# Kernel optimization log

Hardware: AMD Instinct MI355X
Metric: run time of the kernel (lower is better)

Reference implementation:

```python
import jax, jax.numpy as jnp
import numpy as np

B, S, P, V, E, H = 64, 1024, 32, 32000, 128, 256


def _lstm_dir(x, Wih, Whh, b, reverse):
    # x: [S, B, E] -> hidden states [S, B, H]; PyTorch LSTM gate order i,f,g,o
    Bsz = x.shape[1]
    Hd = Whh.shape[1]

    def step(carry, xt):
        h, c = carry
        z = xt @ Wih.T + h @ Whh.T + b
        i, f, g, o = jnp.split(z, 4, axis=-1)
        i = jax.nn.sigmoid(i)
        f = jax.nn.sigmoid(f)
        g = jnp.tanh(g)
        o = jax.nn.sigmoid(o)
        c = f * c + i * g
        h = o * jnp.tanh(c)
        return (h, c), h

    init = (jnp.zeros((Bsz, Hd), x.dtype), jnp.zeros((Bsz, Hd), x.dtype))
    _, hs = jax.lax.scan(step, init, x, reverse=reverse)
    return hs


def setup_inputs():
    key = jax.random.key(0)
    ks = jax.random.split(key, 12)
    input_ids = jax.random.randint(ks[0], (B, S), 0, V)
    attention_mask = jnp.ones((B, S), jnp.int32)
    # token j covers chars [4j, 4j+4)
    starts = jnp.arange(S) * 4
    offset_mapping = jnp.broadcast_to(jnp.stack([starts, starts + 4], -1), (B, S, 2))
    # spans: contiguous token runs of 1..64 tokens, expressed as char offsets
    t0 = jax.random.randint(ks[1], (B, P), 0, S - 64)
    ln = jax.random.randint(ks[2], (B, P), 1, 64)
    positions = jnp.stack([t0 * 4, (t0 + ln) * 4], -1)
    sc = 0.05
    embedding = (jax.random.normal(ks[3], (V, E)) * sc).at[0].set(0.0)  # padding_idx=0
    Wih_f = jax.random.normal(ks[4], (4 * H, E)) * sc
    Whh_f = jax.random.normal(ks[5], (4 * H, H)) * sc
    bih_f = jnp.zeros((4 * H,))
    bhh_f = jnp.zeros((4 * H,))
    Wih_b = jax.random.normal(ks[6], (4 * H, E)) * sc
    Whh_b = jax.random.normal(ks[7], (4 * H, H)) * sc
    bih_b = jnp.zeros((4 * H,))
    bhh_b = jnp.zeros((4 * H,))
    fc_w = jax.random.normal(ks[8], (1, 2 * H)) * sc
    fc_b = jnp.zeros((1,))
    return dict(embedding=embedding, Wih_f=Wih_f, Whh_f=Whh_f, bih_f=bih_f, bhh_f=bhh_f,
                Wih_b=Wih_b, Whh_b=Whh_b, bih_b=bih_b, bhh_b=bhh_b, fc_w=fc_w, fc_b=fc_b,
                input_ids=input_ids, attention_mask=attention_mask,
                offset_mapping=offset_mapping, positions=positions)


def reference(embedding, Wih_f, Whh_f, bih_f, bhh_f, Wih_b, Whh_b, bih_b, bhh_b,
              fc_w, fc_b, input_ids, attention_mask, offset_mapping, positions):
    x = embedding[input_ids]              # [B,S,E]
    xt = jnp.swapaxes(x, 0, 1)            # [S,B,E]
    h_f = _lstm_dir(xt, Wih_f, Whh_f, bih_f + bhh_f, False)
    h_b = _lstm_dir(xt, Wih_b, Whh_b, bih_b + bhh_b, True)
    lstm_out = jnp.swapaxes(jnp.concatenate([h_f, h_b], -1), 0, 1)  # [B,S,2H]

    off_s = offset_mapping[..., 0]        # [B,S]
    off_e = offset_mapping[..., 1]
    pos_s = positions[..., 0]             # [B,P]
    pos_e = positions[..., 1]
    # token j belongs to span p iff s_j >= start_p and e_j <= end_p
    mask = (off_s[:, None, :] >= pos_s[:, :, None]) & (off_e[:, None, :] <= pos_e[:, :, None])
    m = mask.astype(lstm_out.dtype)       # [B,P,S]
    cnt = m.sum(-1)                       # [B,P]
    reps = jnp.einsum('bps,bsd->bpd', m, lstm_out) / jnp.maximum(cnt, 1.0)[..., None]
    valid = (cnt > 0) & ~((pos_s == 0) & (pos_e == 0))
    reps = jnp.where(valid[..., None], reps, 0.0)
    logits = reps @ fc_w.T + fc_b         # [B,P,1]
    return logits.squeeze(-1)
```

## Files before the change

kernel.cpp:

```cpp
#include <hip/hip_runtime.h>

#define S_  1024
#define B_  64
#define P_  32

typedef _Float16 f16;
typedef unsigned int u32;
typedef _Float16 half2_t __attribute__((ext_vector_type(2)));
typedef _Float16 half8_t __attribute__((ext_vector_type(8)));

__device__ __forceinline__ float dot8(half8_t w, half8_t h, float acc) {
#if __has_builtin(__builtin_amdgcn_fdot2)
    acc = __builtin_amdgcn_fdot2((half2_t){w[0], w[1]}, (half2_t){h[0], h[1]}, acc, false);
    acc = __builtin_amdgcn_fdot2((half2_t){w[2], w[3]}, (half2_t){h[2], h[3]}, acc, false);
    acc = __builtin_amdgcn_fdot2((half2_t){w[4], w[5]}, (half2_t){h[4], h[5]}, acc, false);
    acc = __builtin_amdgcn_fdot2((half2_t){w[6], w[7]}, (half2_t){h[6], h[7]}, acc, false);
#else
    #pragma unroll
    for (int j = 0; j < 8; ++j) acc += (float)w[j] * (float)h[j];
#endif
    return acc;
}

__device__ __forceinline__ float fast_sig(float x)  { return 1.f / (1.f + __expf(-x)); }
__device__ __forceinline__ float fast_tanh(float x) { return 1.f - 2.f / (1.f + __expf(2.f * x)); }

__global__ void k_prep_w(const float* __restrict__ wih_f, const float* __restrict__ whh_f,
                         const float* __restrict__ bih_f, const float* __restrict__ bhh_f,
                         const float* __restrict__ wih_b, const float* __restrict__ whh_b,
                         const float* __restrict__ bih_b, const float* __restrict__ bhh_b,
                         f16* __restrict__ Wreg, f16* __restrict__ Wlds,
                         float* __restrict__ bias2) {
    int rowg = blockIdx.x;
    int dir = rowg >> 10;
    int r = rowg & 1023;
    int col = threadIdx.x;
    int g = r >> 8, rem = r & 255, half = rem >> 7, up = rem & 127;
    int rid = g * 128 + up;
    const float* wih = dir ? wih_b : wih_f;
    const float* whh = dir ? whh_b : whh_f;
    if (col < 128) {
        float v = wih[r * 128 + col];
        Wreg[((((size_t)(dir * 2 + half) * 2 + 0) * 16 + (col >> 3)) * 512 + rid) * 8 + (col & 7)] = (f16)v;
    } else {
        int k = col - 128;
        float v = whh[r * 256 + k];
        int hc = k >> 7, kk = k & 127, c = kk >> 3, j = kk & 7;
        if (hc == half)
            Wreg[((((size_t)(dir * 2 + half) * 2 + 1) * 16 + c) * 512 + rid) * 8 + j] = (f16)v;
        else
            Wlds[(((size_t)(dir * 2 + half) * 16 + c) * 512 + rid) * 8 + j] = (f16)v;
    }
    if (col == 0) {
        const float* bi = dir ? bih_b : bih_f;
        const float* bh = dir ? bhh_b : bhh_f;
        bias2[rowg] = bi[r] + bh[r];
    }
}

__global__ void k_gather(const int* __restrict__ ids, const float* __restrict__ emb,
                         f16* __restrict__ X) {
    int m = blockIdx.x * 2 + (threadIdx.x >> 7);
    int k = threadIdx.x & 127;
    int id = ids[m];
    X[(size_t)m * 128 + k] = (f16)emb[(size_t)id * 128 + k];
}

__global__ void k_zero(u32* __restrict__ flags) {
    flags[threadIdx.x] = 0u;
}

__global__ __launch_bounds__(512, 1) void k_lstm(
        const f16* __restrict__ Wreg,
        const f16* __restrict__ Wlds,
        const float* __restrict__ bias2,
        const f16* __restrict__ X,
        const float* __restrict__ fcw,
        f16* __restrict__ Hx,
        u32* __restrict__ flags,
        float* __restrict__ Svp) {
    __shared__ __align__(16) f16 sh_w[16 * 512 * 8];
    __shared__ __align__(16) f16 sh_h[256];
    __shared__ float zbuf[4][128];

    const int blk  = blockIdx.x;
    const int dir  = blk >> 7;
    const int half = (blk >> 6) & 1;
    const int b    = blk & 63;
    const int tid  = threadIdx.x;
    const int g    = tid >> 7;
    const int up   = tid & 127;
    const int row  = g * 256 + half * 128 + up;

    const half8_t* wrg = (const half8_t*)Wreg;
    const size_t base_x = (((size_t)(dir * 2 + half) * 2 + 0) * 16) * 512 + tid;
    const size_t base_h = (((size_t)(dir * 2 + half) * 2 + 1) * 16) * 512 + tid;
    half8_t wx[16], wh[16];
    #pragma unroll
    for (int c = 0; c < 16; ++c) wx[c] = wrg[base_x + (size_t)c * 512];
    #pragma unroll
    for (int c = 0; c < 16; ++c) wh[c] = wrg[base_h + (size_t)c * 512];

    {
        const half8_t* wlg = (const half8_t*)Wlds + ((size_t)(dir * 2 + half) * 16) * 512 + tid;
        half8_t* shw = (half8_t*)sh_w;
        #pragma unroll
        for (int c = 0; c < 16; ++c) shw[c * 512 + tid] = wlg[(size_t)c * 512];
    }

    const float bias = bias2[dir * 1024 + row];

    const f16* Xb = X + (size_t)b * S_ * 128;
    const int fidx_own = (dir * 64 + b) * 2 + half;
    const int fidx_par = fidx_own ^ 1;
    f16*       hx_own = Hx + (size_t)fidx_own * 2 * 128;
    const f16* hx_par = Hx + (size_t)fidx_par * 2 * 128;

    float c0 = 0.f, c1 = 0.f, fc0 = 0.f, fc1 = 0.f;
    if (tid < 64) {
        fc0 = fcw[dir * 256 + half * 128 + 2 * tid];
        fc1 = fcw[dir * 256 + half * 128 + 2 * tid + 1];
    }

    if (tid < 128) ((u32*)sh_h)[tid] = 0u;
    __syncthreads();

    const half8_t* shh = (const half8_t*)sh_h;
    const half8_t* shw = (const half8_t*)sh_w;
    const int ownc = half * 16;
    const int parc = (1 - half) * 16;

    for (int s = 0; s < S_; ++s) {
        const int t = dir ? (S_ - 1 - s) : s;
        const half8_t* xrow = (const half8_t*)&Xb[(size_t)t * 128];

        float a0 = 0.f, a1 = 0.f, a2 = 0.f, a3 = 0.f;

        #pragma unroll
        for (int c = 0; c < 16; c += 2) {
            a0 = dot8(wh[c],     shh[ownc + c],     a0);
            a1 = dot8(wh[c + 1], shh[ownc + c + 1], a1);
        }
        #pragma unroll
        for (int c = 0; c < 16; c += 2) {
            a2 = dot8(wx[c],     xrow[c],     a2);
            a3 = dot8(wx[c + 1], xrow[c + 1], a3);
        }

        if (s > 0 && tid < 64) {
            if (tid == 0) {
                while (__hip_atomic_load(&flags[fidx_par], __ATOMIC_ACQUIRE,
                                         __HIP_MEMORY_SCOPE_AGENT) < (u32)s)
                    __builtin_amdgcn_s_sleep(1);
            }
            if (tid < 16)
                *(half8_t*)&sh_h[(1 - half) * 128 + tid * 8] =
                    *(const half8_t*)&hx_par[(size_t)(s & 1) * 128 + tid * 8];
        }
        __syncthreads();

        #pragma unroll
        for (int c = 0; c < 16; c += 2) {
            half8_t w0 = shw[c * 512 + tid];
            half8_t w1 = shw[(c + 1) * 512 + tid];
            a0 = dot8(w0, shh[parc + c],     a0);
            a1 = dot8(w1, shh[parc + c + 1], a1);
        }

        float z = a0 + a1 + a2 + a3 + bias;
        float act = (g == 2) ? fast_tanh(z) : fast_sig(z);
        zbuf[g][up] = act;
        __syncthreads();

        if (tid < 64) {
            const int u0 = 2 * tid, u1 = u0 + 1;
            float i0 = zbuf[0][u0], f0 = zbuf[1][u0], g0 = zbuf[2][u0], o0 = zbuf[3][u0];
            float i1 = zbuf[0][u1], f1 = zbuf[1][u1], g1 = zbuf[2][u1], o1 = zbuf[3][u1];
            c0 = f0 * c0 + i0 * g0;
            c1 = f1 * c1 + i1 * g1;
            float h0 = o0 * fast_tanh(c0);
            float h1 = o1 * fast_tanh(c1);
            f16 h0h = (f16)h0, h1h = (f16)h1;
            u32 packed = (u32)__builtin_bit_cast(unsigned short, h0h)
                       | ((u32)__builtin_bit_cast(unsigned short, h1h) << 16);
            ((u32*)&sh_h[half * 128])[tid] = packed;
            ((u32*)&hx_own[(size_t)((s + 1) & 1) * 128])[tid] = packed;
            float ps = h0 * fc0 + h1 * fc1;
            #pragma unroll
            for (int off = 32; off > 0; off >>= 1) ps += __shfl_down(ps, off);
            if (tid == 0) {
                __hip_atomic_store(&flags[fidx_own], (u32)(s + 1), __ATOMIC_RELEASE,
                                   __HIP_MEMORY_SCOPE_AGENT);
                Svp[(((size_t)half * 2 + dir) * 64 + b) * S_ + t] = ps;
            }
        }
        __syncthreads();
    }
}

__global__ __launch_bounds__(256) void k_pool(const float* __restrict__ Svp,
                                              const int* __restrict__ om,
                                              const int* __restrict__ pos,
                                              const float* __restrict__ fcb,
                                              float* __restrict__ out) {
    __shared__ float red[4][2];
    int bp = blockIdx.x;
    int b = bp >> 5, p = bp & 31;
    int ps = pos[(b * P_ + p) * 2];
    int pe = pos[(b * P_ + p) * 2 + 1];
    int tid = threadIdx.x;
    float sum = 0.f, cnt = 0.f;
    for (int j = tid; j < S_; j += 256) {
        int os = om[((size_t)b * S_ + j) * 2];
        int oe = om[((size_t)b * S_ + j) * 2 + 1];
        if (os >= ps && oe <= pe) {
            size_t base = (size_t)b * S_ + j;
            sum += Svp[0 * 65536 + base] + Svp[1 * 65536 + base]
                 + Svp[2 * 65536 + base] + Svp[3 * 65536 + base];
            cnt += 1.f;
        }
    }
    #pragma unroll
    for (int off = 32; off > 0; off >>= 1) {
        sum += __shfl_down(sum, off);
        cnt += __shfl_down(cnt, off);
    }
    if ((tid & 63) == 0) { red[tid >> 6][0] = sum; red[tid >> 6][1] = cnt; }
    __syncthreads();
    if (tid == 0) {
        sum = red[0][0] + red[1][0] + red[2][0] + red[3][0];
        cnt = red[0][1] + red[1][1] + red[2][1] + red[3][1];
        bool valid = (cnt > 0.f) && !(ps == 0 && pe == 0);
        float v = valid ? (sum / fmaxf(cnt, 1.f)) : 0.f;
        out[b * P_ + p] = v + fcb[0];
    }
}

extern "C" void kernel_launch(void* const* d_in, const int* in_sizes, int n_in,
                              void* d_out, int out_size, void* d_ws, size_t ws_size,
                              hipStream_t stream) {
    const float* emb   = (const float*)d_in[0];
    const float* wih_f = (const float*)d_in[1];
    const float* whh_f = (const float*)d_in[2];
    const float* bih_f = (const float*)d_in[3];
    const float* bhh_f = (const float*)d_in[4];
    const float* wih_b = (const float*)d_in[5];
    const float* whh_b = (const float*)d_in[6];
    const float* bih_b = (const float*)d_in[7];
    const float* bhh_b = (const float*)d_in[8];
    const float* fc_w  = (const float*)d_in[9];
    const float* fc_b  = (const float*)d_in[10];
    const int* ids     = (const int*)d_in[11];
    const int* om      = (const int*)d_in[13];
    const int* pos     = (const int*)d_in[14];

    char* ws = (char*)d_ws;
    f16*   X     = (f16*)(ws + 0);
    f16*   Wreg  = (f16*)(ws + 16777216);
    f16*   Wlds  = (f16*)(ws + 17825792);
    float* bias2 = (float*)(ws + 18350080);
    f16*   Hx    = (f16*)(ws + 18358272);
    u32*   flags = (u32*)(ws + 18489344);
    float* Svp   = (float*)(ws + 18490368);
    float* out   = (float*)d_out;

    k_prep_w<<<2048, 384, 0, stream>>>(wih_f, whh_f, bih_f, bhh_f,
                                       wih_b, whh_b, bih_b, bhh_b, Wreg, Wlds, bias2);
    k_gather<<<32768, 256, 0, stream>>>(ids, emb, X);
    k_zero<<<1, 256, 0, stream>>>(flags);
    k_lstm<<<256, 512, 0, stream>>>(Wreg, Wlds, bias2, X, fc_w, Hx, flags, Svp);
    k_pool<<<2048, 256, 0, stream>>>(Svp, om, pos, fc_b, out);
}
```

Before: 8.117 ms.

## Split LSTM gate dot products across 1024 threads and batch input projections per 32 steps

Each block now runs 1024 threads, with each pair of threads splitting the K dimension of a gate row. All recurrent weights are held in registers, so the LDS weight copy goes away. The input projection W_x·x_t is computed in chunks of 32 timesteps into an LDS buffer stored as fp16, which takes the x loads and the dot products off the per-step critical path. The cost is an extra barrier per step to combine the partial sums, and fp16 rounding of the input projection.

```diff
diff --git a/kernel.cpp b/kernel.cpp
--- a/kernel.cpp
+++ b/kernel.cpp
@@ -29,27 +29,26 @@
                          const float* __restrict__ bih_f, const float* __restrict__ bhh_f,
                          const float* __restrict__ wih_b, const float* __restrict__ whh_b,
                          const float* __restrict__ bih_b, const float* __restrict__ bhh_b,
-                         f16* __restrict__ Wreg, f16* __restrict__ Wlds,
+                         f16* __restrict__ Whh_sw, f16* __restrict__ Wx_sw,
                          float* __restrict__ bias2) {
     int rowg = blockIdx.x;
     int dir = rowg >> 10;
     int r = rowg & 1023;
     int col = threadIdx.x;
-    int g = r >> 8, rem = r & 255, half = rem >> 7, up = rem & 127;
-    int rid = g * 128 + up;
+    int g = r >> 8, half = (r >> 7) & 1, u = r & 127;
+    int rloc = g * 128 + u;
     const float* wih = dir ? wih_b : wih_f;
     const float* whh = dir ? whh_b : whh_f;
     if (col < 128) {
-        float v = wih[r * 128 + col];
-        Wreg[((((size_t)(dir * 2 + half) * 2 + 0) * 16 + (col >> 3)) * 512 + rid) * 8 + (col & 7)] = (f16)v;
+        int q = col >> 6, c = (col >> 3) & 7, j = col & 7;
+        Wx_sw[(((((size_t)dir * 2 + half) * 2 + q) * 8 + c) * 512 + rloc) * 8 + j] =
+            (f16)wih[r * 128 + col];
     } else {
-        int k = col - 128;
-        float v = whh[r * 256 + k];
-        int hc = k >> 7, kk = k & 127, c = kk >> 3, j = kk & 7;
-        if (hc == half)
-            Wreg[((((size_t)(dir * 2 + half) * 2 + 1) * 16 + c) * 512 + rid) * 8 + j] = (f16)v;
-        else
-            Wlds[(((size_t)(dir * 2 + half) * 16 + c) * 512 + rid) * 8 + j] = (f16)v;
+        int v = col - 128;
+        int cc = v >> 3, j = v & 7;
+        int q = cc & 1, cp = cc >> 1;
+        Whh_sw[(((((size_t)dir * 2 + half) * 2 + q) * 16 + cp) * 512 + rloc) * 8 + j] =
+            (f16)whh[r * 256 + v];
     }
     if (col == 0) {
         const float* bi = dir ? bih_b : bih_f;
@@ -70,45 +69,35 @@
     flags[threadIdx.x] = 0u;
 }
 
-__global__ __launch_bounds__(512, 1) void k_lstm(
-        const f16* __restrict__ Wreg,
-        const f16* __restrict__ Wlds,
+__global__ __launch_bounds__(1024, 1) void k_lstm(
+        const f16* __restrict__ Whh_sw,
+        const f16* __restrict__ Wx_sw,
         const float* __restrict__ bias2,
         const f16* __restrict__ X,
         const float* __restrict__ fcw,
         f16* __restrict__ Hx,
         u32* __restrict__ flags,
         float* __restrict__ Svp) {
-    __shared__ __align__(16) f16 sh_w[16 * 512 * 8];
+    __shared__ __align__(16) f16 zxp[2][512][38];
     __shared__ __align__(16) f16 sh_h[256];
-    __shared__ float zbuf[4][128];
+    __shared__ float zbuf[512];
+    __shared__ float zpart[512];
 
     const int blk  = blockIdx.x;
     const int dir  = blk >> 7;
     const int half = (blk >> 6) & 1;
     const int b    = blk & 63;
     const int tid  = threadIdx.x;
-    const int g    = tid >> 7;
-    const int up   = tid & 127;
-    const int row  = g * 256 + half * 128 + up;
-
-    const half8_t* wrg = (const half8_t*)Wreg;
-    const size_t base_x = (((size_t)(dir * 2 + half) * 2 + 0) * 16) * 512 + tid;
-    const size_t base_h = (((size_t)(dir * 2 + half) * 2 + 1) * 16) * 512 + tid;
-    half8_t wx[16], wh[16];
+    const int q    = tid >> 9;
+    const int r    = tid & 511;
+    const int g    = r >> 7;
+
+    const half8_t* whp = (const half8_t*)Whh_sw + ((((size_t)dir * 2 + half) * 2 + q) * 16) * 512 + r;
+    half8_t wh[16];
     #pragma unroll
-    for (int c = 0; c < 16; ++c) wx[c] = wrg[base_x + (size_t)c * 512];
-    #pragma unroll
-    for (int c = 0; c < 16; ++c) wh[c] = wrg[base_h + (size_t)c * 512];
-
-    {
-        const half8_t* wlg = (const half8_t*)Wlds + ((size_t)(dir * 2 + half) * 16) * 512 + tid;
-        half8_t* shw = (half8_t*)sh_w;
-        #pragma unroll
-        for (int c = 0; c < 16; ++c) shw[c * 512 + tid] = wlg[(size_t)c * 512];
-    }
-
-    const float bias = bias2[dir * 1024 + row];
+    for (int c = 0; c < 16; ++c) wh[c] = whp[(size_t)c * 512];
+
+    const float bias = bias2[dir * 1024 + g * 256 + half * 128 + (r & 127)];
 
     const f16* Xb = X + (size_t)b * S_ * 128;
     const int fidx_own = (dir * 64 + b) * 2 + half;
@@ -116,7 +105,7 @@
     f16*       hx_own = Hx + (size_t)fidx_own * 2 * 128;
     const f16* hx_par = Hx + (size_t)fidx_par * 2 * 128;
 
-    float c0 = 0.f, c1 = 0.f, fc0 = 0.f, fc1 = 0.f;
+    float cs0 = 0.f, cs1 = 0.f, fc0 = 0.f, fc1 = 0.f;
     if (tid < 64) {
         fc0 = fcw[dir * 256 + half * 128 + 2 * tid];
         fc1 = fcw[dir * 256 + half * 128 + 2 * tid + 1];
@@ -125,27 +114,41 @@
     if (tid < 128) ((u32*)sh_h)[tid] = 0u;
     __syncthreads();
 
-    const half8_t* shh = (const half8_t*)sh_h;
-    const half8_t* shw = (const half8_t*)sh_w;
-    const int ownc = half * 16;
-    const int parc = (1 - half) * 16;
+    const int c_own = half * 8;
+    const int c_par = 8 - half * 8;
 
     for (int s = 0; s < S_; ++s) {
+        if ((s & 31) == 0) {
+            const half8_t* wxp = (const half8_t*)Wx_sw +
+                ((((size_t)dir * 2 + half) * 2 + q) * 8) * 512 + r;
+            half8_t wx[8];
+            #pragma unroll
+            for (int c = 0; c < 8; ++c) wx[c] = wxp[(size_t)c * 512];
+            for (int tp = 0; tp < 32; tp += 2) {
+                int t0 = dir ? (S_ - 1 - (s + tp)) : (s + tp);
+                int t1 = dir ? (t0 - 1) : (t0 + 1);
+                const half8_t* x0 = (const half8_t*)&Xb[(size_t)t0 * 128] + q * 8;
+                const half8_t* x1 = (const half8_t*)&Xb[(size_t)t1 * 128] + q * 8;
+                float a0 = 0.f, a1 = 0.f;
+                #pragma unroll
+                for (int c = 0; c < 8; ++c) {
+                    a0 = dot8(wx[c], x0[c], a0);
+                    a1 = dot8(wx[c], x1[c], a1);
+                }
+                f16 p0 = (f16)a0, p1 = (f16)a1;
+                u32 pk = (u32)__builtin_bit_cast(unsigned short, p0)
+                       | ((u32)__builtin_bit_cast(unsigned short, p1) << 16);
+                *(u32*)&zxp[q][r][tp] = pk;
+            }
+            __syncthreads();
+        }
+
         const int t = dir ? (S_ - 1 - s) : s;
-        const half8_t* xrow = (const half8_t*)&Xb[(size_t)t * 128];
-
-        float a0 = 0.f, a1 = 0.f, a2 = 0.f, a3 = 0.f;
+        float acc = 0.f;
 
         #pragma unroll
-        for (int c = 0; c < 16; c += 2) {
-            a0 = dot8(wh[c],     shh[ownc + c],     a0);
-            a1 = dot8(wh[c + 1], shh[ownc + c + 1], a1);
-        }
-        #pragma unroll
-        for (int c = 0; c < 16; c += 2) {
-            a2 = dot8(wx[c],     xrow[c],     a2);
-            a3 = dot8(wx[c + 1], xrow[c + 1], a3);
-        }
+        for (int c = 0; c < 8; ++c)
+            acc = dot8(wh[c_own + c], *(const half8_t*)&sh_h[(2 * (c_own + c) + q) * 8], acc);
 
         if (s > 0 && tid < 64) {
             if (tid == 0) {
@@ -160,26 +163,30 @@
         __syncthreads();
 
         #pragma unroll
-        for (int c = 0; c < 16; c += 2) {
-            half8_t w0 = shw[c * 512 + tid];
-            half8_t w1 = shw[(c + 1) * 512 + tid];
-            a0 = dot8(w0, shh[parc + c],     a0);
-            a1 = dot8(w1, shh[parc + c + 1], a1);
-        }
-
-        float z = a0 + a1 + a2 + a3 + bias;
-        float act = (g == 2) ? fast_tanh(z) : fast_sig(z);
-        zbuf[g][up] = act;
+        for (int c = 0; c < 8; ++c)
+            acc = dot8(wh[c_par + c], *(const half8_t*)&sh_h[(2 * (c_par + c) + q) * 8], acc);
+
+        if (q == 1) zpart[r] = acc;
+        __syncthreads();
+
+        if (q == 0) {
+            float zx0 = (float)zxp[0][r][s & 31];
+            float zx1 = (float)zxp[1][r][s & 31];
+            float z = acc + zpart[r] + zx0 + zx1 + bias;
+            zbuf[r] = (g == 2) ? fast_tanh(z) : fast_sig(z);
+        }
         __syncthreads();
 
         if (tid < 64) {
-            const int u0 = 2 * tid, u1 = u0 + 1;
-            float i0 = zbuf[0][u0], f0 = zbuf[1][u0], g0 = zbuf[2][u0], o0 = zbuf[3][u0];
-            float i1 = zbuf[0][u1], f1 = zbuf[1][u1], g1 = zbuf[2][u1], o1 = zbuf[3][u1];
-            c0 = f0 * c0 + i0 * g0;
-            c1 = f1 * c1 + i1 * g1;
-            float h0 = o0 * fast_tanh(c0);
-            float h1 = o1 * fast_tanh(c1);
+            const float2* zb2 = (const float2*)zbuf;
+            float2 iv = zb2[tid];
+            float2 fv = zb2[64 + tid];
+            float2 gv = zb2[128 + tid];
+            float2 ov = zb2[192 + tid];
+            cs0 = fv.x * cs0 + iv.x * gv.x;
+            cs1 = fv.y * cs1 + iv.y * gv.y;
+            float h0 = ov.x * fast_tanh(cs0);
+            float h1 = ov.y * fast_tanh(cs1);
             f16 h0h = (f16)h0, h1h = (f16)h1;
             u32 packed = (u32)__builtin_bit_cast(unsigned short, h0h)
                        | ((u32)__builtin_bit_cast(unsigned short, h1h) << 16);
@@ -255,19 +262,19 @@
     const int* pos     = (const int*)d_in[14];
 
     char* ws = (char*)d_ws;
-    f16*   X     = (f16*)(ws + 0);
-    f16*   Wreg  = (f16*)(ws + 16777216);
-    f16*   Wlds  = (f16*)(ws + 17825792);
-    float* bias2 = (float*)(ws + 18350080);
-    f16*   Hx    = (f16*)(ws + 18358272);
-    u32*   flags = (u32*)(ws + 18489344);
-    float* Svp   = (float*)(ws + 18490368);
-    float* out   = (float*)d_out;
+    f16*   X      = (f16*)(ws + 0);
+    f16*   WhhSw  = (f16*)(ws + 16777216);
+    f16*   WxSw   = (f16*)(ws + 18874368);
+    float* bias2  = (float*)(ws + 19922944);
+    f16*   Hx     = (f16*)(ws + 19931136);
+    u32*   flags  = (u32*)(ws + 20062208);
+    float* Svp    = (float*)(ws + 20063232);
+    float* out    = (float*)d_out;
 
     k_prep_w<<<2048, 384, 0, stream>>>(wih_f, whh_f, bih_f, bhh_f,
-                                       wih_b, whh_b, bih_b, bhh_b, Wreg, Wlds, bias2);
+                                       wih_b, whh_b, bih_b, bhh_b, WhhSw, WxSw, bias2);
     k_gather<<<32768, 256, 0, stream>>>(ids, emb, X);
     k_zero<<<1, 256, 0, stream>>>(flags);
-    k_lstm<<<256, 512, 0, stream>>>(Wreg, Wlds, bias2, X, fc_w, Hx, flags, Svp);
+    k_lstm<<<256, 1024, 0, stream>>>(WhhSw, WxSw, bias2, X, fc_w, Hx, flags, Svp);
     k_pool<<<2048, 256, 0, stream>>>(Svp, om, pos, fc_b, out);
 }
```

New measurement: 17.49 ms. 2.15x slower.
